# Kernel optimization log

Measured on AMD Instinct MI355X. Metric: run time of the kernel, lower is better.

The kernel has to match this reference:

```python
import jax, jax.numpy as jnp
import numpy as np
import math

IMAGE_SIZE = 300
STEPS = [16, 32, 64, 100, 150, 300]
MIN_SIZES = [60, 105, 150, 195, 240, 285]
MAX_SIZES = [105, 150, 195, 240, 285, 330]
ASPECT_RATIOS = [2, 3]
SCORE_THRESH = 0.02
NMS_THRESH = 0.45
POST_NMS_TOP_N = 100
VAR_XY, VAR_WH = 0.1, 0.2
BATCH, NUM_CLASSES = 16, 201


def _make_priors():
    # SSD-style anchor generation in (cx, cy, w, h), relative coords.
    priors = []
    for k, step in enumerate(STEPS):
        f = math.ceil(IMAGE_SIZE / step)
        s = MIN_SIZES[k] / IMAGE_SIZE
        sp = math.sqrt(MIN_SIZES[k] * MAX_SIZES[k]) / IMAGE_SIZE
        for i in range(f):
            for j in range(f):
                cx = (j + 0.5) * step / IMAGE_SIZE
                cy = (i + 0.5) * step / IMAGE_SIZE
                priors.append([cx, cy, s, s])
                priors.append([cx, cy, sp, sp])
                for ar in ASPECT_RATIOS:
                    r = math.sqrt(ar)
                    priors.append([cx, cy, s * r, s / r])
                    priors.append([cx, cy, s / r, s * r])
    return np.asarray(priors, dtype=np.float32)  # [3000, 4]


def setup_inputs() -> dict:
    key = jax.random.key(0)
    k1, k2 = jax.random.split(key)
    priors = jnp.asarray(_make_priors())  # [P, 4]
    P = priors.shape[0]
    pred_bbox_deltas = jax.random.normal(k1, (BATCH, P, 4), dtype=jnp.float32)
    objectness = jax.random.normal(k2, (BATCH, P, NUM_CLASSES), dtype=jnp.float32)
    return {"pred_bbox_deltas": pred_bbox_deltas, "objectness": objectness, "priors": priors}


def reference(pred_bbox_deltas, objectness, priors):
    # Eval path of MultiBoxHeads.filter_priors: softmax -> box decode ->
    # score filter -> class-aware (batched) NMS -> top-N, padded to fixed size.
    P = priors.shape[0]
    C = objectness.shape[-1]
    probs = jax.nn.softmax(objectness, axis=-1)  # [B, P, C]

    # BoxCoder.decode with variances (0.1, 0.2); priors are (cx, cy, w, h).
    pxy, pwh = priors[:, :2], priors[:, 2:]
    xy = pred_bbox_deltas[..., :2] * VAR_XY * pwh + pxy  # [B, P, 2]
    wh = jnp.exp(pred_bbox_deltas[..., 2:] * VAR_WH) * pwh
    decoded = jnp.concatenate([xy - 0.5 * wh, xy + 0.5 * wh], axis=-1)  # [B, P, 4] xyxy

    # Per-candidate class labels (background class 0 dropped), shared across images.
    labels = jnp.broadcast_to(jnp.arange(1, C), (P, C - 1)).reshape(-1)  # [P*(C-1)] int

    def nms_image(dec, prob):
        scores = prob[:, 1:].reshape(-1)  # [P*(C-1)]
        boxes = jnp.broadcast_to(dec[:, None, :], (P, C - 1, 4)).reshape(-1, 4)
        s = jnp.where(scores > SCORE_THRESH, scores, -1.0)
        # batched_nms trick: offset boxes by label so classes never overlap.
        off = jnp.max(boxes) + 1.0
        bo = boxes + labels.astype(boxes.dtype)[:, None] * off
        areas = (bo[:, 2] - bo[:, 0]) * (bo[:, 3] - bo[:, 1])

        def step(s, _):
            i = jnp.argmax(s)
            sc = s[i]
            b = bo[i]
            ix1 = jnp.maximum(bo[:, 0], b[0])
            iy1 = jnp.maximum(bo[:, 1], b[1])
            ix2 = jnp.minimum(bo[:, 2], b[2])
            iy2 = jnp.minimum(bo[:, 3], b[3])
            inter = jnp.clip(ix2 - ix1, 0.0) * jnp.clip(iy2 - iy1, 0.0)
            iou = inter / (areas + areas[i] - inter)
            s = jnp.where(iou > NMS_THRESH, -1.0, s).at[i].set(-1.0)
            return s, (i, sc)

        _, (idx, sc) = jax.lax.scan(step, s, None, length=POST_NMS_TOP_N)
        ok = sc > SCORE_THRESH  # slots that hold real detections
        b_out = jnp.where(ok[:, None], jnp.clip(boxes[idx], 0.0, 1.0), 0.0)  # parse() clamp
        s_out = jnp.where(ok, sc, 0.0)
        l_out = jnp.where(ok, labels[idx].astype(boxes.dtype), 0.0)
        # [K, 6] = (x1, y1, x2, y2, score, label); zero rows are padding.
        return jnp.concatenate([b_out, s_out[:, None], l_out[:, None]], axis=-1)

    return jax.vmap(nms_image)(decoded, probs)  # [B, POST_NMS_TOP_N, 6]
```

## Files before the change

kernel.cpp:

```cpp
#include <hip/hip_runtime.h>
#include <cfloat>
#include <cstdint>

#define BATCH 16
#define PRIORS 3000
#define NCLS 201
#define NLBL 200
#define TOPN 100
#define SCORE_THR 0.02f
#define NMS_THR 0.45f

#define FPPB 16
#define FBLK ((PRIORS + FPPB - 1) / FPPB)
#define SEGW 64
#define SEGS (FBLK * 4)
#define SLOTS (SEGS * SEGW)
#define HOTW 8
#define OVF_CAP 1024
#define T0 0.08f

#define NMS_T 1024
#define NBINS 1024
#define HCAP 512
#define ADJS 514
#define SB_BASE 0x3CA3

__device__ __forceinline__ int key_stratum(uint64_t k) {
    int s = (int)(k >> 48) - SB_BASE;
    return s < 0 ? 0 : (s > NBINS - 1 ? NBINS - 1 : s);
}

__global__ __launch_bounds__(256) void score_filter_kernel(
    const float* __restrict__ obj,
    int*         __restrict__ cnt,
    int*         __restrict__ hcnt,
    uint64_t*    __restrict__ seg,
    uint64_t*    __restrict__ hot,
    uint64_t*    __restrict__ ovf,
    uint64_t*    __restrict__ hovf)
{
    const int b    = blockIdx.y;
    const int wave = threadIdx.x >> 6;
    const int lane = threadIdx.x & 63;
    const int segId = blockIdx.x * 4 + wave;
    uint64_t* myseg = seg + ((size_t)b * SEGS + segId) * SEGW;
    uint64_t* myhot = hot + ((size_t)b * SEGS + segId) * HOTW;
    const int pbase = blockIdx.x * FPPB + wave * 4;

    float v0[4], v1[4], v2[4], v3[4];
    bool pv[4];
#pragma unroll
    for (int pp = 0; pp < 4; ++pp) {
        int p = pbase + pp;
        pv[pp] = (p < PRIORS);
        const float* x = obj + ((size_t)b * PRIORS + (pv[pp] ? p : PRIORS - 1)) * NCLS;
        v0[pp] = x[lane];
        v1[pp] = x[lane + 64];
        v2[pp] = x[lane + 128];
        v3[pp] = (lane + 192 < NCLS) ? x[lane + 192] : -FLT_MAX;
    }
    float mx[4];
#pragma unroll
    for (int pp = 0; pp < 4; ++pp)
        mx[pp] = fmaxf(fmaxf(v0[pp], v1[pp]), fmaxf(v2[pp], v3[pp]));
    for (int d = 32; d > 0; d >>= 1) {
#pragma unroll
        for (int pp = 0; pp < 4; ++pp)
            mx[pp] = fmaxf(mx[pp], __shfl_xor(mx[pp], d, 64));
    }
    float e0[4], e1[4], e2[4], e3[4], se[4];
#pragma unroll
    for (int pp = 0; pp < 4; ++pp) {
        e0[pp] = expf(v0[pp] - mx[pp]);
        e1[pp] = expf(v1[pp] - mx[pp]);
        e2[pp] = expf(v2[pp] - mx[pp]);
        e3[pp] = (lane + 192 < NCLS) ? expf(v3[pp] - mx[pp]) : 0.0f;
        se[pp] = e0[pp] + e1[pp] + e2[pp] + e3[pp];
    }
    for (int d = 32; d > 0; d >>= 1) {
#pragma unroll
        for (int pp = 0; pp < 4; ++pp)
            se[pp] += __shfl_xor(se[pp], d, 64);
    }
    int cursor = 0, hcur = 0;
#pragma unroll
    for (int pp = 0; pp < 4; ++pp) {
        float inv = 1.0f / se[pp];
        int p = pbase + pp;
        float ev[4] = { e0[pp], e1[pp], e2[pp], e3[pp] };
#pragma unroll
        for (int k = 0; k < 4; ++k) {
            int c = lane + 64 * k;
            float prob = ev[k] * inv;
            bool pass = pv[pp] && (c >= 1) && (c < NCLS) && (prob > SCORE_THR);
            uint64_t mask = __ballot(pass);
            bool hotp = pass && (prob > T0);
            uint64_t hmask = __ballot(hotp);
            if (pass) {
                uint32_t oid = (uint32_t)(p * NLBL + (c - 1));
                uint64_t key = ((uint64_t)__float_as_uint(prob) << 32)
                             | (uint64_t)(0xFFFFFFFFu - oid);
                int idx = cursor + __popcll(mask & ((1ull << lane) - 1ull));
                if (idx < SEGW) {
                    myseg[idx] = key;
                } else {
                    int gi = atomicAdd(&cnt[b], 1);
                    if (gi < OVF_CAP) ovf[(size_t)b * OVF_CAP + gi] = key;
                }
                if (hotp) {
                    int hidx = hcur + __popcll(hmask & ((1ull << lane) - 1ull));
                    if (hidx < HOTW) {
                        myhot[hidx] = key;
                    } else {
                        int gi = atomicAdd(&hcnt[b], 1);
                        if (gi < OVF_CAP) hovf[(size_t)b * OVF_CAP + gi] = key;
                    }
                }
            }
            cursor += (int)__popcll(mask);
            hcur   += (int)__popcll(hmask);
        }
    }
    if (lane >= (cursor < SEGW ? cursor : SEGW)) myseg[lane] = 0ull;
    if (lane < HOTW && lane >= (hcur < HOTW ? hcur : HOTW)) myhot[lane] = 0ull;
}

__device__ __forceinline__ void sort512_desc(const uint64_t* skey,
                                             uint64_t K[8], int lane)
{
#pragma unroll
    for (int r = 0; r < 8; ++r) K[r] = skey[r * 64 + lane];
#pragma unroll
    for (int k2 = 2; k2 <= 512; k2 <<= 1) {
#pragma unroll
        for (int j2 = k2 >> 1; j2 >= 64; j2 >>= 1) {
            int j2r = j2 >> 6;
#pragma unroll
            for (int r = 0; r < 8; ++r) {
                if ((r & j2r) == 0) {
                    int rp = r | j2r;
                    bool up = ((((r << 6) + lane) & k2) == 0);
                    uint64_t a = K[r], bb = K[rp];
                    uint64_t mxk = a > bb ? a : bb;
                    uint64_t mnk = a > bb ? bb : a;
                    K[r]  = up ? mxk : mnk;
                    K[rp] = up ? mnk : mxk;
                }
            }
        }
#pragma unroll
        for (int j2 = ((k2 >> 1) < 32 ? (k2 >> 1) : 32); j2 >= 1; j2 >>= 1) {
#pragma unroll
            for (int r = 0; r < 8; ++r) {
                uint64_t o = __shfl_xor((unsigned long long)K[r], j2, 64);
                bool up = ((((r << 6) + lane) & k2) == 0);
                bool lower = ((lane & j2) == 0);
                K[r] = (up == lower) ? (K[r] > o ? K[r] : o)
                                     : (K[r] < o ? K[r] : o);
            }
        }
    }
}

__device__ __forceinline__ int scan_sorted_w0(
    const uint64_t K[8], int b, const float4* __restrict__ dbox, float ofb,
    float4* abox, float* aarea, int na, float* __restrict__ out, int lane)
{
#pragma unroll
    for (int r = 0; r < 8; ++r) {
        if (na >= TOPN) break;
        uint64_t myk = K[r];
        bool valid = (myk != 0ull);
        uint32_t oid = 0xFFFFFFFFu - (uint32_t)myk;
        int p = valid ? (int)(oid / NLBL) : 0;
        int c = valid ? ((int)(oid - (uint32_t)p * NLBL) + 1) : 1;
        float4 db = dbox[p];
        float lof = (float)c * ofb;
        float qx1 = db.x + lof, qy1 = db.y + lof;
        float qx2 = db.z + lof, qy2 = db.w + lof;
        float aq = (qx2 - qx1) * (qy2 - qy1);
        bool dead = false;
        for (int l = 0; l < na; ++l) {
            float4 a = abox[l];
            float ix1 = fmaxf(qx1, a.x), iy1 = fmaxf(qy1, a.y);
            float ix2 = fminf(qx2, a.z), iy2 = fminf(qy2, a.w);
            float inter = fmaxf(ix2 - ix1, 0.0f) * fmaxf(iy2 - iy1, 0.0f);
            float iou = inter / (aq + aarea[l] - inter);
            if (iou > NMS_THR) dead = true;
        }
        uint64_t alive = __ballot(valid && !dead);
        while (alive != 0ull && na < TOPN) {
            int j = __ffsll((unsigned long long)alive) - 1;
            float ax1 = __shfl(qx1, j, 64);
            float ay1 = __shfl(qy1, j, 64);
            float ax2 = __shfl(qx2, j, 64);
            float ay2 = __shfl(qy2, j, 64);
            float aa  = __shfl(aq,  j, 64);
            if (lane == j) {
                abox[na]  = make_float4(qx1, qy1, qx2, qy2);
                aarea[na] = aq;
                float* o = out + ((size_t)b * TOPN + na) * 6;
                o[0] = fminf(fmaxf(db.x, 0.0f), 1.0f);
                o[1] = fminf(fmaxf(db.y, 0.0f), 1.0f);
                o[2] = fminf(fmaxf(db.z, 0.0f), 1.0f);
                o[3] = fminf(fmaxf(db.w, 0.0f), 1.0f);
                o[4] = __uint_as_float((uint32_t)(myk >> 32));
                o[5] = (float)c;
            }
            na++;
            bool mine = ((alive >> lane) & 1ull) != 0ull;
            bool drop = (lane == j);
            if (mine && !drop) {
                float ix1 = fmaxf(qx1, ax1), iy1 = fmaxf(qy1, ay1);
                float ix2 = fminf(qx2, ax2), iy2 = fminf(qy2, ay2);
                float inter = fmaxf(ix2 - ix1, 0.0f) * fmaxf(iy2 - iy1, 0.0f);
                float iou = inter / (aq + aa - inter);
                if (iou > NMS_THR) drop = true;
            }
            alive = __ballot(mine && !drop);
        }
    }
    return na;
}

__device__ __forceinline__ int scan_step_w0(
    uint64_t key, int b, const float4* __restrict__ dbox, float ofb,
    float4* abox, float* aarea, int na, float* __restrict__ out, int lane)
{
    uint32_t oid = 0xFFFFFFFFu - (uint32_t)key;
    int p = (int)(oid / NLBL);
    int c = (int)(oid - (uint32_t)p * NLBL) + 1;
    float4 db = dbox[p];
    float lo = (float)c * ofb;
    float qx1 = db.x + lo, qy1 = db.y + lo;
    float qx2 = db.z + lo, qy2 = db.w + lo;
    float aq = (qx2 - qx1) * (qy2 - qy1);
    bool sup = false;
    for (int l = lane; l < na; l += 64) {
        float4 a = abox[l];
        float ix1 = fmaxf(qx1, a.x), iy1 = fmaxf(qy1, a.y);
        float ix2 = fminf(qx2, a.z), iy2 = fminf(qy2, a.w);
        float inter = fmaxf(ix2 - ix1, 0.0f) * fmaxf(iy2 - iy1, 0.0f);
        float iou = inter / (aq + aarea[l] - inter);
        if (iou > NMS_THR) sup = true;
    }
    if (__ballot(sup) == 0ull) {
        if (lane == 0) {
            abox[na]  = make_float4(qx1, qy1, qx2, qy2);
            aarea[na] = aq;
            float* o = out + ((size_t)b * TOPN + na) * 6;
            o[0] = fminf(fmaxf(db.x, 0.0f), 1.0f);
            o[1] = fminf(fmaxf(db.y, 0.0f), 1.0f);
            o[2] = fminf(fmaxf(db.z, 0.0f), 1.0f);
            o[3] = fminf(fmaxf(db.w, 0.0f), 1.0f);
            o[4] = __uint_as_float((uint32_t)(key >> 32));
            o[5] = (float)c;
        }
        __threadfence_block();
        return na + 1;
    }
    return na;
}

__global__ __launch_bounds__(NMS_T) void nms_kernel(
    const float*    __restrict__ deltas,
    const float*    __restrict__ priors,
    const int*      __restrict__ cnt,
    const int*      __restrict__ hcnt,
    const uint64_t* __restrict__ seg,
    const uint64_t* __restrict__ hot,
    const uint64_t* __restrict__ ovf,
    const uint64_t* __restrict__ hovf,
    float*          __restrict__ out)
{
    __shared__ float4   dbox[PRIORS];
    __shared__ int      sufx[NBINS];
    __shared__ uint64_t skey[HCAP];
    __shared__ float4   qbox[HCAP];
    __shared__ float    qarea[HCAP];
    __shared__ uint64_t adjT[8 * ADJS];
    __shared__ float4   abox[112];
    __shared__ float    aarea[112];
    __shared__ uint64_t rk[NMS_T / 64];
    __shared__ float    wredF[NMS_T / 64];
    __shared__ int      wtotS[NMS_T / 64];
    __shared__ int      carryS[NMS_T / 64];
    __shared__ int cntC, loS, naS;
    __shared__ uint64_t fkS;

    const int b    = blockIdx.x;
    const int tid  = threadIdx.x;
    const int wave = tid >> 6;
    const int lane = tid & 63;
    const uint64_t* slots  = seg  + (size_t)b * SLOTS;
    const uint64_t* hslots = hot  + (size_t)b * SEGS * HOTW;
    int n_ovf  = cnt[b];  if (n_ovf  > OVF_CAP) n_ovf  = OVF_CAP;
    int n_hovf = hcnt[b]; if (n_hovf > OVF_CAP) n_hovf = OVF_CAP;
    const uint64_t* ovfp  = ovf  + (size_t)b * OVF_CAP;
    const uint64_t* hovfp = hovf + (size_t)b * OVF_CAP;

    if (tid == 0) { cntC = 0; naS = 0; }
    if (lane == 0) wredF[wave] = -FLT_MAX;
    __syncthreads();

    for (int j = tid; j < SEGS * HOTW; j += NMS_T) {
        uint64_t k = hslots[j];
        if (k) { int i = atomicAdd(&cntC, 1); if (i < HCAP) skey[i] = k; }
    }
    for (int j = tid; j < n_hovf; j += NMS_T) {
        uint64_t k = hovfp[j];
        if (k) { int i = atomicAdd(&cntC, 1); if (i < HCAP) skey[i] = k; }
    }
    __syncthreads();
    int hc = cntC;
    bool decoded = false;
    if (hc <= HCAP) {
        if (tid < HCAP && tid >= hc) skey[tid] = 0ull;
        __syncthreads();
        if (wave == 0) {
            uint64_t K[8];
            sort512_desc(skey, K, lane);
#pragma unroll
            for (int r = 0; r < 8; ++r) skey[r * 64 + lane] = K[r];
        } else {
            int base0 = (wave - 1) * 200;
            float lmax = -FLT_MAX;
            for (int p = base0 + lane; p < base0 + 200; p += 64) {
                float4 d4 = ((const float4*)deltas)[(size_t)b * PRIORS + p];
                float4 pr = ((const float4*)priors)[p];
                float cx = d4.x * 0.1f * pr.z + pr.x;
                float cy = d4.y * 0.1f * pr.w + pr.y;
                float w  = expf(d4.z * 0.2f) * pr.z;
                float h  = expf(d4.w * 0.2f) * pr.w;
                float x1 = cx - 0.5f * w, y1 = cy - 0.5f * h;
                float x2 = cx + 0.5f * w, y2 = cy + 0.5f * h;
                dbox[p] = make_float4(x1, y1, x2, y2);
                lmax = fmaxf(lmax, fmaxf(fmaxf(x1, y1), fmaxf(x2, y2)));
            }
            for (int d = 32; d > 0; d >>= 1)
                lmax = fmaxf(lmax, __shfl_xor(lmax, d, 64));
            if (lane == 0) wredF[wave] = lmax;
        }
        decoded = true;
        __syncthreads();

        float v = wredF[lane & 15];
        for (int d = 8; d > 0; d >>= 1) v = fmaxf(v, __shfl_xor(v, d, 64));
        float ofb = v + 1.0f;

        if (tid < HCAP) {
            uint64_t k = skey[tid];
            bool valid = (k != 0ull);
            uint32_t oid = 0xFFFFFFFFu - (uint32_t)k;
            int p = valid ? (int)(oid / NLBL) : 0;
            int c = valid ? ((int)(oid - (uint32_t)p * NLBL) + 1) : 1;
            float4 db = dbox[p];
            float lof = (float)c * ofb;
            float4 q = make_float4(db.x + lof, db.y + lof,
                                   db.z + lof, db.w + lof);
            qbox[tid]  = q;
            qarea[tid] = (q.z - q.x) * (q.w - q.y);
        }
        for (int i = tid; i < 8 * ADJS; i += NMS_T) adjT[i] = 0ull;
        __syncthreads();

        int hcw = (hc + 63) >> 6;
        int P2  = (hcw * (hcw + 1)) >> 1;
        for (int tau = tid; tau < (P2 << 6); tau += NMS_T) {
            int pair = tau >> 6, rr = tau & 63;
            int w = 0;
            while ((((w + 1) * (w + 2)) >> 1) <= pair) ++w;
            int cw = pair - ((w * (w + 1)) >> 1);
            int r  = (cw << 6) + rr;
            float4 qr = qbox[r];
            float  ar = qarea[r];
            int jb = w << 6;
            uint64_t m = 0ull;
#pragma unroll 8
            for (int j = 0; j < 64; ++j) {
                float4 qj = qbox[jb + j];
                float ix1 = fmaxf(qr.x, qj.x), iy1 = fmaxf(qr.y, qj.y);
                float ix2 = fminf(qr.z, qj.z), iy2 = fminf(qr.w, qj.w);
                float inter = fmaxf(ix2 - ix1, 0.0f) * fmaxf(iy2 - iy1, 0.0f);
                float iou = inter / (ar + qarea[jb + j] - inter);
                m |= (uint64_t)(iou > NMS_THR) << j;
            }
            if (w == cw) m &= ~((1ull << rr) - 1ull);
            adjT[w * ADJS + r] = m;
        }
        if (wave == 0 && lane < 8) rk[lane] = 0ull;
        __syncthreads();

        if (wave == 0) {
            uint64_t sup = 0ull;
            int na = 0;
            for (int w = 0; w < hcw && na < TOPN; ++w) {
                int nInW = hc - (w << 6);
                uint64_t init = (nInW >= 64) ? ~0ull
                              : (nInW > 0 ? ((1ull << nInW) - 1ull) : 0ull);
                uint64_t supw = (uint64_t)__shfl((long long)sup, 8 + w, 64);
                uint64_t rem  = init & ~supw;
                uint64_t accw = 0ull;
                while (rem != 0ull && na < TOPN) {
                    int rr = __ffsll((unsigned long long)rem) - 1;
                    int r  = (w << 6) + rr;
                    accw |= 1ull << rr;
                    uint64_t rowk = 0ull;
                    if (lane >= 8 && lane < 16)
                        rowk = adjT[(lane - 8) * ADJS + r];
                    sup |= rowk;
                    rem &= ~adjT[w * ADJS + r];
                    ++na;
                }
                if (lane == 0) rk[w] = accw;
            }
            if (lane == 0) naS = na;
        }
        __syncthreads();

        if (tid < HCAP) {
            int w = tid >> 6, rr = tid & 63;
            uint64_t aw = rk[w];
            if ((aw >> rr) & 1ull) {
                int idx = (int)__popcll(aw & ((1ull << rr) - 1ull));
                for (int k = 0; k < w; ++k) idx += (int)__popcll(rk[k]);
                uint64_t myk = skey[tid];
                uint32_t oid = 0xFFFFFFFFu - (uint32_t)myk;
                int p = (int)(oid / NLBL);
                int c = (int)(oid - (uint32_t)p * NLBL) + 1;
                float4 db = dbox[p];
                float* o = out + ((size_t)b * TOPN + idx) * 6;
                o[0] = fminf(fmaxf(db.x, 0.0f), 1.0f);
                o[1] = fminf(fmaxf(db.y, 0.0f), 1.0f);
                o[2] = fminf(fmaxf(db.z, 0.0f), 1.0f);
                o[3] = fminf(fmaxf(db.w, 0.0f), 1.0f);
                o[4] = __uint_as_float((uint32_t)(myk >> 32));
                o[5] = (float)c;
            }
        }
        __syncthreads();
    }

    if (naS < TOPN) {
        if (!decoded) {
            float lmax = -FLT_MAX;
            for (int p = tid; p < PRIORS; p += NMS_T) {
                float4 d4 = ((const float4*)deltas)[(size_t)b * PRIORS + p];
                float4 pr = ((const float4*)priors)[p];
                float cx = d4.x * 0.1f * pr.z + pr.x;
                float cy = d4.y * 0.1f * pr.w + pr.y;
                float w  = expf(d4.z * 0.2f) * pr.z;
                float h  = expf(d4.w * 0.2f) * pr.w;
                float x1 = cx - 0.5f * w, y1 = cy - 0.5f * h;
                float x2 = cx + 0.5f * w, y2 = cy + 0.5f * h;
                dbox[p] = make_float4(x1, y1, x2, y2);
                lmax = fmaxf(lmax, fmaxf(fmaxf(x1, y1), fmaxf(x2, y2)));
            }
            for (int d = 32; d > 0; d >>= 1)
                lmax = fmaxf(lmax, __shfl_xor(lmax, d, 64));
            if (lane == 0) wredF[wave] = lmax;
        }
        sufx[tid] = 0;
        if (tid == 0) naS = 0;
        __syncthreads();
        for (int j = tid; j < SLOTS; j += NMS_T) {
            uint64_t k = slots[j];
            if (k) atomicAdd(&sufx[key_stratum(k)], 1);
        }
        for (int j = tid; j < n_ovf; j += NMS_T) {
            uint64_t k = ovfp[j];
            if (k) atomicAdd(&sufx[key_stratum(k)], 1);
        }
        __syncthreads();
        {
            int v = sufx[64 * wave + lane];
            int s = v;
            for (int d = 1; d < 64; d <<= 1) {
                int t = __shfl_down(s, d, 64);
                if (lane + d < 64) s += t;
            }
            if (lane == 0) wtotS[wave] = s;
            __syncthreads();
            if (wave == 0 && lane < NMS_T / 64) {
                int tv = wtotS[lane];
                int ts = tv;
                for (int d = 1; d < NMS_T / 64; d <<= 1) {
                    int t = __shfl_down(ts, d, 64);
                    if (lane + d < NMS_T / 64) ts += t;
                }
                carryS[lane] = ts - tv;
            }
            __syncthreads();
            sufx[64 * wave + lane] = s + carryS[wave];
        }
        int curHi = NBINS;
        for (;;) {
            __syncthreads();
            int naCur = naS;
            int A = (curHi < NBINS) ? sufx[curHi] : 0;
            int remaining = sufx[0] - A;
            if (naCur >= TOPN || remaining <= 0 || curHi <= 0) break;
            int target = A + HCAP;
            if (tid == 0) { loS = curHi; cntC = 0; }
            __syncthreads();
            if (tid < curHi) {
                if (sufx[tid] <= target && (tid == 0 || sufx[tid - 1] > target))
                    loS = tid;
            }
            __syncthreads();
            int lo = loS;

            if (lo < curHi) {
                for (int j = tid; j < SLOTS; j += NMS_T) {
                    uint64_t k = slots[j];
                    if (k) {
                        int s = key_stratum(k);
                        if (s >= lo && s < curHi) {
                            int i = atomicAdd(&cntC, 1);
                            if (i < HCAP) skey[i] = k;
                        }
                    }
                }
                for (int j = tid; j < n_ovf; j += NMS_T) {
                    uint64_t k = ovfp[j];
                    if (k) {
                        int s = key_stratum(k);
                        if (s >= lo && s < curHi) {
                            int i = atomicAdd(&cntC, 1);
                            if (i < HCAP) skey[i] = k;
                        }
                    }
                }
                __syncthreads();
                if (tid < HCAP && tid >= cntC) skey[tid] = 0ull;
                __syncthreads();
                if (wave == 0) {
                    uint64_t K[8];
                    sort512_desc(skey, K, lane);
                    float ofb;
                    {
                        float v = (lane < NMS_T / 64) ? wredF[lane] : -FLT_MAX;
                        for (int d = 32; d > 0; d >>= 1) v = fmaxf(v, __shfl_xor(v, d, 64));
                        ofb = v + 1.0f;
                    }
                    int na = scan_sorted_w0(K, b, dbox, ofb, abox, aarea, naS, out, lane);
                    if (lane == 0) naS = na;
                }
                curHi = lo;
            } else {
                float ofbT;
                {
                    float v = (lane < NMS_T / 64) ? wredF[lane] : -FLT_MAX;
                    for (int d = 32; d > 0; d >>= 1) v = fmaxf(v, __shfl_xor(v, d, 64));
                    ofbT = v + 1.0f;
                }
                int s = curHi - 1;
                uint64_t lastK = ~0ull;
                for (;;) {
                    __syncthreads();
                    if (naS >= TOPN) break;
                    uint64_t bk = 0ull;
                    for (int j = tid; j < SLOTS; j += NMS_T) {
                        uint64_t k = slots[j];
                        if (k && key_stratum(k) == s && k < lastK && k > bk) bk = k;
                    }
                    for (int j = tid; j < n_ovf; j += NMS_T) {
                        uint64_t k = ovfp[j];
                        if (k && key_stratum(k) == s && k < lastK && k > bk) bk = k;
                    }
                    for (int d = 32; d > 0; d >>= 1) {
                        uint64_t o = __shfl_xor((unsigned long long)bk, d, 64);
                        bk = (o > bk) ? o : bk;
                    }
                    if (lane == 0) rk[wave] = bk;
                    __syncthreads();
                    if (tid == 0) {
                        uint64_t fk = rk[0];
                        for (int w = 1; w < NMS_T / 64; ++w) fk = (rk[w] > fk) ? rk[w] : fk;
                        fkS = fk;
                    }
                    __syncthreads();
                    uint64_t fk = fkS;
                    if (fk == 0ull) break;
                    if (wave == 0) {
                        int nal = naS;
                        nal = scan_step_w0(fk, b, dbox, ofbT, abox, aarea, nal, out, lane);
                        if (lane == 0) naS = nal;
                    }
                    lastK = fk;
                }
                curHi = s;
            }
        }
    }
    __syncthreads();
    int naF = naS;
    for (int idx = tid; idx < (TOPN - naF) * 6; idx += NMS_T)
        out[(size_t)b * TOPN * 6 + (size_t)naF * 6 + idx] = 0.0f;
}

extern "C" void kernel_launch(void* const* d_in, const int* in_sizes, int n_in,
                              void* d_out, int out_size, void* d_ws, size_t ws_size,
                              hipStream_t stream)
{
    const float* deltas = (const float*)d_in[0];
    const float* obj    = (const float*)d_in[1];
    const float* priors = (const float*)d_in[2];
    float* out = (float*)d_out;

    char* ws = (char*)d_ws;
    int*      cnt  = (int*)ws;
    int*      hcnt = (int*)(ws + 64);
    uint64_t* hotA = (uint64_t*)(ws + 256);
    uint64_t* segA = hotA + (size_t)BATCH * SEGS * HOTW;
    uint64_t* ovfA = segA + (size_t)BATCH * SLOTS;
    uint64_t* hovA = ovfA + (size_t)BATCH * OVF_CAP;

    hipMemsetAsync(ws, 0, 128, stream);
    dim3 fg(FBLK, BATCH, 1);
    score_filter_kernel<<<fg, 256, 0, stream>>>(obj, cnt, hcnt, segA, hotA, ovfA, hovA);
    nms_kernel<<<BATCH, NMS_T, 0, stream>>>(deltas, priors, cnt, hcnt,
                                            segA, hotA, ovfA, hovA, out);
}
```

Before: 134.0 us.

## Compact hot candidates via per-wave atomics and transpose NMS suppression matrix

The score filter now appends hot candidates (prob > T0) to a compact per-image list, using one wave-level atomicAdd per ballot, instead of writing fixed per-segment hot slots plus an overflow buffer. The NMS kernel then reads that list directly, which removes the compaction scan over all hot slots and its shared-memory atomics. The IoU adjacency matrix is stored column-wise, so each lane owns one candidate and the greedy selection inside a 64-wide word uses a ballot per step instead of dependent shared-memory row loads. The cost is global atomic contention in the filter kernel and a nondeterministic candidate order before the sort.

```diff
diff --git a/kernel.cpp b/kernel.cpp
--- a/kernel.cpp
+++ b/kernel.cpp
@@ -15,14 +15,13 @@
 #define SEGW 64
 #define SEGS (FBLK * 4)
 #define SLOTS (SEGS * SEGW)
-#define HOTW 8
 #define OVF_CAP 1024
+#define HOT_CAP 1024
 #define T0 0.08f
 
 #define NMS_T 1024
 #define NBINS 1024
 #define HCAP 512
-#define ADJS 514
 #define SB_BASE 0x3CA3
 
 __device__ __forceinline__ int key_stratum(uint64_t k) {
@@ -35,16 +34,14 @@
     int*         __restrict__ cnt,
     int*         __restrict__ hcnt,
     uint64_t*    __restrict__ seg,
-    uint64_t*    __restrict__ hot,
-    uint64_t*    __restrict__ ovf,
-    uint64_t*    __restrict__ hovf)
+    uint64_t*    __restrict__ hotC,
+    uint64_t*    __restrict__ ovf)
 {
     const int b    = blockIdx.y;
     const int wave = threadIdx.x >> 6;
     const int lane = threadIdx.x & 63;
     const int segId = blockIdx.x * 4 + wave;
     uint64_t* myseg = seg + ((size_t)b * SEGS + segId) * SEGW;
-    uint64_t* myhot = hot + ((size_t)b * SEGS + segId) * HOTW;
     const int pbase = blockIdx.x * FPPB + wave * 4;
 
     float v0[4], v1[4], v2[4], v3[4];
@@ -82,7 +79,7 @@
         for (int pp = 0; pp < 4; ++pp)
             se[pp] += __shfl_xor(se[pp], d, 64);
     }
-    int cursor = 0, hcur = 0;
+    int cursor = 0;
 #pragma unroll
     for (int pp = 0; pp < 4; ++pp) {
         float inv = 1.0f / se[pp];
@@ -96,6 +93,12 @@
             uint64_t mask = __ballot(pass);
             bool hotp = pass && (prob > T0);
             uint64_t hmask = __ballot(hotp);
+            int hbase = 0;
+            if (hmask) {
+                if (lane == 0)
+                    hbase = atomicAdd(&hcnt[b], (int)__popcll(hmask));
+                hbase = __shfl(hbase, 0, 64);
+            }
             if (pass) {
                 uint32_t oid = (uint32_t)(p * NLBL + (c - 1));
                 uint64_t key = ((uint64_t)__float_as_uint(prob) << 32)
@@ -108,21 +111,15 @@
                     if (gi < OVF_CAP) ovf[(size_t)b * OVF_CAP + gi] = key;
                 }
                 if (hotp) {
-                    int hidx = hcur + __popcll(hmask & ((1ull << lane) - 1ull));
-                    if (hidx < HOTW) {
-                        myhot[hidx] = key;
-                    } else {
-                        int gi = atomicAdd(&hcnt[b], 1);
-                        if (gi < OVF_CAP) hovf[(size_t)b * OVF_CAP + gi] = key;
-                    }
+                    int hi = hbase + (int)__popcll(hmask & ((1ull << lane) - 1ull));
+                    if (hi < HOT_CAP)
+                        hotC[(size_t)b * HOT_CAP + hi] = key;
                 }
             }
             cursor += (int)__popcll(mask);
-            hcur   += (int)__popcll(hmask);
         }
     }
     if (lane >= (cursor < SEGW ? cursor : SEGW)) myseg[lane] = 0ull;
-    if (lane < HOTW && lane >= (hcur < HOTW ? hcur : HOTW)) myhot[lane] = 0ull;
 }
 
 __device__ __forceinline__ void sort512_desc(const uint64_t* skey,
@@ -268,9 +265,8 @@
     const int*      __restrict__ cnt,
     const int*      __restrict__ hcnt,
     const uint64_t* __restrict__ seg,
-    const uint64_t* __restrict__ hot,
+    const uint64_t* __restrict__ hotC,
     const uint64_t* __restrict__ ovf,
-    const uint64_t* __restrict__ hovf,
     float*          __restrict__ out)
 {
     __shared__ float4   dbox[PRIORS];
@@ -278,7 +274,7 @@
     __shared__ uint64_t skey[HCAP];
     __shared__ float4   qbox[HCAP];
     __shared__ float    qarea[HCAP];
-    __shared__ uint64_t adjT[8 * ADJS];
+    __shared__ uint64_t adjB[8 * HCAP];
     __shared__ float4   abox[112];
     __shared__ float    aarea[112];
     __shared__ uint64_t rk[NMS_T / 64];
@@ -292,30 +288,19 @@
     const int tid  = threadIdx.x;
     const int wave = tid >> 6;
     const int lane = tid & 63;
-    const uint64_t* slots  = seg  + (size_t)b * SLOTS;
-    const uint64_t* hslots = hot  + (size_t)b * SEGS * HOTW;
-    int n_ovf  = cnt[b];  if (n_ovf  > OVF_CAP) n_ovf  = OVF_CAP;
-    int n_hovf = hcnt[b]; if (n_hovf > OVF_CAP) n_hovf = OVF_CAP;
-    const uint64_t* ovfp  = ovf  + (size_t)b * OVF_CAP;
-    const uint64_t* hovfp = hovf + (size_t)b * OVF_CAP;
+    const uint64_t* slots = seg  + (size_t)b * SLOTS;
+    const uint64_t* hotp_ = hotC + (size_t)b * HOT_CAP;
+    int n_ovf = cnt[b]; if (n_ovf > OVF_CAP) n_ovf = OVF_CAP;
+    const uint64_t* ovfp = ovf + (size_t)b * OVF_CAP;
 
     if (tid == 0) { cntC = 0; naS = 0; }
     if (lane == 0) wredF[wave] = -FLT_MAX;
     __syncthreads();
 
-    for (int j = tid; j < SEGS * HOTW; j += NMS_T) {
-        uint64_t k = hslots[j];
-        if (k) { int i = atomicAdd(&cntC, 1); if (i < HCAP) skey[i] = k; }
-    }
-    for (int j = tid; j < n_hovf; j += NMS_T) {
-        uint64_t k = hovfp[j];
-        if (k) { int i = atomicAdd(&cntC, 1); if (i < HCAP) skey[i] = k; }
-    }
-    __syncthreads();
-    int hc = cntC;
+    int hc = hcnt[b];
     bool decoded = false;
     if (hc <= HCAP) {
-        if (tid < HCAP && tid >= hc) skey[tid] = 0ull;
+        if (tid < HCAP) skey[tid] = (tid < hc) ? hotp_[tid] : 0ull;
         __syncthreads();
         if (wave == 0) {
             uint64_t K[8];
@@ -361,58 +346,63 @@
             qbox[tid]  = q;
             qarea[tid] = (q.z - q.x) * (q.w - q.y);
         }
-        for (int i = tid; i < 8 * ADJS; i += NMS_T) adjT[i] = 0ull;
+        for (int i = tid; i < 8 * HCAP; i += NMS_T) adjB[i] = 0ull;
         __syncthreads();
 
         int hcw = (hc + 63) >> 6;
         int P2  = (hcw * (hcw + 1)) >> 1;
-        for (int tau = tid; tau < (P2 << 6); tau += NMS_T) {
-            int pair = tau >> 6, rr = tau & 63;
-            int w = 0;
-            while ((((w + 1) * (w + 2)) >> 1) <= pair) ++w;
-            int cw = pair - ((w * (w + 1)) >> 1);
-            int r  = (cw << 6) + rr;
-            float4 qr = qbox[r];
-            float  ar = qarea[r];
-            int jb = w << 6;
+        for (int pair = wave; pair < P2; pair += NMS_T / 64) {
+            int wj = 0;
+            while ((((wj + 1) * (wj + 2)) >> 1) <= pair) ++wj;
+            int wi = pair - ((wj * (wj + 1)) >> 1);
+            int j  = (wj << 6) + lane;
+            float4 qj = qbox[j];
+            float  aj = qarea[j];
+            int ib = wi << 6;
             uint64_t m = 0ull;
 #pragma unroll 8
-            for (int j = 0; j < 64; ++j) {
-                float4 qj = qbox[jb + j];
-                float ix1 = fmaxf(qr.x, qj.x), iy1 = fmaxf(qr.y, qj.y);
-                float ix2 = fminf(qr.z, qj.z), iy2 = fminf(qr.w, qj.w);
+            for (int i = 0; i < 64; ++i) {
+                float4 qi = qbox[ib + i];
+                float ix1 = fmaxf(qj.x, qi.x), iy1 = fmaxf(qj.y, qi.y);
+                float ix2 = fminf(qj.z, qi.z), iy2 = fminf(qj.w, qi.w);
                 float inter = fmaxf(ix2 - ix1, 0.0f) * fmaxf(iy2 - iy1, 0.0f);
-                float iou = inter / (ar + qarea[jb + j] - inter);
-                m |= (uint64_t)(iou > NMS_THR) << j;
-            }
-            if (w == cw) m &= ~((1ull << rr) - 1ull);
-            adjT[w * ADJS + r] = m;
+                float iou = inter / (aj + qarea[ib + i] - inter);
+                m |= (uint64_t)(iou > NMS_THR) << i;
+            }
+            if (wi == wj)
+                m &= (lane == 63) ? ~0ull : ((1ull << (lane + 1)) - 1ull);
+            adjB[wi * HCAP + j] = m;
         }
         if (wave == 0 && lane < 8) rk[lane] = 0ull;
         __syncthreads();
 
         if (wave == 0) {
-            uint64_t sup = 0ull;
+            uint64_t accwA[8];
+#pragma unroll
+            for (int w = 0; w < 8; ++w) accwA[w] = 0ull;
             int na = 0;
-            for (int w = 0; w < hcw && na < TOPN; ++w) {
-                int nInW = hc - (w << 6);
-                uint64_t init = (nInW >= 64) ? ~0ull
-                              : (nInW > 0 ? ((1ull << nInW) - 1ull) : 0ull);
-                uint64_t supw = (uint64_t)__shfl((long long)sup, 8 + w, 64);
-                uint64_t rem  = init & ~supw;
-                uint64_t accw = 0ull;
-                while (rem != 0ull && na < TOPN) {
-                    int rr = __ffsll((unsigned long long)rem) - 1;
-                    int r  = (w << 6) + rr;
-                    accw |= 1ull << rr;
-                    uint64_t rowk = 0ull;
-                    if (lane >= 8 && lane < 16)
-                        rowk = adjT[(lane - 8) * ADJS + r];
-                    sup |= rowk;
-                    rem &= ~adjT[w * ADJS + r];
-                    ++na;
-                }
-                if (lane == 0) rk[w] = accw;
+#pragma unroll
+            for (int w = 0; w < 8; ++w) {
+                if (w < hcw && na < TOPN) {
+                    int nInW = hc - (w << 6);
+                    uint64_t init = (nInW >= 64) ? ~0ull
+                                  : (nInW > 0 ? ((1ull << nInW) - 1ull) : 0ull);
+                    uint64_t deadOr = 0ull;
+#pragma unroll
+                    for (int wp = 0; wp < w; ++wp)
+                        deadOr |= adjB[wp * HCAP + (w << 6) + lane] & accwA[wp];
+                    uint64_t mycol = adjB[w * HCAP + (w << 6) + lane];
+                    uint64_t rem = init & ~__ballot(deadOr != 0ull);
+                    uint64_t acc = 0ull;
+                    while (rem != 0ull && na < TOPN) {
+                        int rr = __ffsll((unsigned long long)rem) - 1;
+                        acc |= 1ull << rr;
+                        ++na;
+                        rem &= ~__ballot(((mycol >> rr) & 1ull) != 0ull);
+                    }
+                    accwA[w] = acc;
+                    if (lane == 0) rk[w] = acc;
+                }
             }
             if (lane == 0) naS = na;
         }
@@ -612,13 +602,12 @@
     int*      cnt  = (int*)ws;
     int*      hcnt = (int*)(ws + 64);
     uint64_t* hotA = (uint64_t*)(ws + 256);
-    uint64_t* segA = hotA + (size_t)BATCH * SEGS * HOTW;
+    uint64_t* segA = hotA + (size_t)BATCH * HOT_CAP;
     uint64_t* ovfA = segA + (size_t)BATCH * SLOTS;
-    uint64_t* hovA = ovfA + (size_t)BATCH * OVF_CAP;
 
     hipMemsetAsync(ws, 0, 128, stream);
     dim3 fg(FBLK, BATCH, 1);
-    score_filter_kernel<<<fg, 256, 0, stream>>>(obj, cnt, hcnt, segA, hotA, ovfA, hovA);
+    score_filter_kernel<<<fg, 256, 0, stream>>>(obj, cnt, hcnt, segA, hotA, ovfA);
     nms_kernel<<<BATCH, NMS_T, 0, stream>>>(deltas, priors, cnt, hcnt,
-                                            segA, hotA, ovfA, hovA, out);
+                                            segA, hotA, ovfA, out);
 }
```

After: 162.5 us. 1.21x slower.
